# Kernel tuning notes

Hardware: AMD Instinct MI355X
Metric: run time of the kernel (lower is better)

## Reference

```python
import jax, jax.numpy as jnp
import numpy as np

B, S, DIM = 2, 2048, 1024
H, W = 16, 256
HD = DIM // H
SCALE = HD ** -0.5


def setup_inputs() -> dict:
    key = jax.random.key(0)
    ks = jax.random.split(key, 9)
    std = DIM ** -0.5
    return {
        "x": jax.random.normal(ks[0], (B, S, DIM), dtype=jnp.float32),
        "Wq": jax.random.normal(ks[1], (DIM, DIM), dtype=jnp.float32) * std,
        "bq": jnp.zeros((DIM,), dtype=jnp.float32),
        "Wk": jax.random.normal(ks[2], (DIM, DIM), dtype=jnp.float32) * std,
        "bk": jnp.zeros((DIM,), dtype=jnp.float32),
        "Wv": jax.random.normal(ks[3], (DIM, DIM), dtype=jnp.float32) * std,
        "bv": jnp.zeros((DIM,), dtype=jnp.float32),
        "Wo": jax.random.normal(ks[4], (DIM, DIM), dtype=jnp.float32) * std,
        "bo": jnp.zeros((DIM,), dtype=jnp.float32),
    }


def reference(x, Wq, bq, Wk, bk, Wv, bv, Wo, bo):
    b, s, dim = x.shape
    q = (x @ Wq + bq).reshape(b, s, H, HD).transpose(0, 2, 1, 3)  # [B,H,S,HD]
    k = (x @ Wk + bk).reshape(b, s, H, HD).transpose(0, 2, 1, 3)
    v = (x @ Wv + bv).reshape(b, s, H, HD).transpose(0, 2, 1, 3)

    scores = jnp.einsum("bhid,bhjd->bhij", q, k) * SCALE  # [B,H,S,S]
    i = jnp.arange(s)[:, None]
    j = jnp.arange(s)[None, :]
    # valid keys: within causal sliding window [i-W+1, i]
    valid = (j <= i) & (j >= i - W + 1)
    scores = jnp.where(valid, scores, -jnp.inf)
    attn = jax.nn.softmax(scores, axis=-1)
    out = jnp.einsum("bhij,bhjd->bhid", attn, v)  # [B,H,S,HD]
    out = out.transpose(0, 2, 1, 3).reshape(b, s, dim)
    return out @ Wo + bo
```

## Files before the change

kernel.cpp:

```cpp
#include <hip/hip_runtime.h>
#include <stdint.h>

typedef __bf16 bf16;
typedef __bf16 bf16x8 __attribute__((ext_vector_type(8)));
typedef float f32x4 __attribute__((ext_vector_type(4)));

#define MFMA16(a, b, c) __builtin_amdgcn_mfma_f32_16x16x32_bf16((a), (b), (c), 0, 0, 0)

__device__ __forceinline__ void ldsdma16(const void* g, void* l) {
  __builtin_amdgcn_global_load_lds((const __attribute__((address_space(1))) void*)g,
                                   (__attribute__((address_space(3))) void*)l, 16, 0, 0);
}

__global__ __launch_bounds__(256) void prep_kernel(const float* __restrict__ x,
                                                   const float* __restrict__ Wq,
                                                   const float* __restrict__ Wk,
                                                   const float* __restrict__ Wv,
                                                   const float* __restrict__ Wo,
                                                   bf16* __restrict__ xb,
                                                   bf16* __restrict__ WT) {
  __shared__ float tile[64][65];
  if (blockIdx.z == 4) {
    const int t = (blockIdx.y * 16 + blockIdx.x) * 256 + threadIdx.x;
#pragma unroll
    for (int i = 0; i < 16; ++i) {
      const int idx = (t + i * 65536) * 4;
      float4 v = *(const float4*)(x + idx);
      union { bf16 h[4]; uint2 u; } p;
      p.h[0] = (bf16)v.x; p.h[1] = (bf16)v.y; p.h[2] = (bf16)v.z; p.h[3] = (bf16)v.w;
      *(uint2*)(xb + idx) = p.u;
    }
    return;
  }
  const float* src = blockIdx.z == 0 ? Wq : blockIdx.z == 1 ? Wk : blockIdx.z == 2 ? Wv : Wo;
  bf16* dst = WT + (size_t)blockIdx.z * 1024 * 1024;
  const int k0 = blockIdx.y * 64, n0 = blockIdx.x * 64;
  const int rr = threadIdx.x >> 6, c = threadIdx.x & 63;
#pragma unroll
  for (int i = 0; i < 16; ++i) {
    int r = i * 4 + rr;
    tile[r][c] = src[(size_t)(k0 + r) * 1024 + n0 + c];
  }
  __syncthreads();
#pragma unroll
  for (int i = 0; i < 16; ++i) {
    int r = i * 4 + rr;
    dst[(size_t)(n0 + r) * 1024 + k0 + c] = (bf16)tile[c][r];
  }
}

__device__ __forceinline__ void stage_half(const bf16* __restrict__ src, int rowbase,
                                           int koff, char* lds, int bufq, int wave,
                                           int lane) {
#pragma unroll
  for (int i = 0; i < 2; ++i) {
    int chunk = i * 512 + wave * 64 + lane;
    int row = chunk >> 3;
    int cg = (chunk & 7) ^ (row & 7);
    ldsdma16(src + (size_t)(rowbase + row) * 1024 + koff + cg * 8,
             lds + bufq * 16384 + (i * 512 + wave * 64) * 16);
  }
}

__device__ __forceinline__ void ld_frag4(const bf16* lds, int bufq, int rbase, int quad,
                                         int l16, bf16x8 (&d)[4][2]) {
  const bf16x8* hb = (const bf16x8*)lds + bufq * 1024;
#pragma unroll
  for (int mf = 0; mf < 4; ++mf) {
    int row = rbase + mf * 16 + l16;
#pragma unroll
    for (int kk = 0; kk < 2; ++kk)
      d[mf][kk] = hb[row * 8 + ((kk * 4 + quad) ^ (row & 7))];
  }
}

__device__ __forceinline__ void ld_frag2(const bf16* lds, int bufq, int rbase, int quad,
                                         int l16, bf16x8 (&d)[2][2]) {
  const bf16x8* hb = (const bf16x8*)lds + bufq * 1024;
#pragma unroll
  for (int nf = 0; nf < 2; ++nf) {
    int row = rbase + nf * 16 + l16;
#pragma unroll
    for (int kk = 0; kk < 2; ++kk)
      d[nf][kk] = hb[row * 8 + ((kk * 4 + quad) ^ (row & 7))];
  }
}

template <int MQ, int NQ>
__device__ __forceinline__ void mma_quad(f32x4 (&acc)[8][4], const bf16x8 (&a)[4][2],
                                         const bf16x8 (&b)[2][2]) {
  __builtin_amdgcn_s_setprio(1);
#pragma unroll
  for (int mf = 0; mf < 4; ++mf)
#pragma unroll
    for (int nf = 0; nf < 2; ++nf)
#pragma unroll
      for (int kk = 0; kk < 2; ++kk)
        acc[MQ * 4 + mf][NQ * 2 + nf] =
            MFMA16(a[mf][kk], b[nf][kk], acc[MQ * 4 + mf][NQ * 2 + nf]);
  __builtin_amdgcn_s_setprio(0);
}

#define QBAR1() { __builtin_amdgcn_s_barrier(); \
                  asm volatile("s_waitcnt lgkmcnt(0)" ::: "memory"); }
#define QBAR2() { __builtin_amdgcn_s_barrier(); }

template <bool PRE>
__device__ __forceinline__ void qkv_iter(int k0, const bf16* __restrict__ xb,
                                         const bf16* __restrict__ BT, int m0, int n0,
                                         bf16* As, bf16* Bs, f32x4 (&acc)[8][4], int wave,
                                         int lane, int wm, int wn, int quad, int l16) {
  bf16x8 aF[4][2], b0F[2][2], b1F[2][2];
  ld_frag4(As, 0, wm * 64, quad, l16, aF);
  ld_frag2(Bs, 0, wn * 32, quad, l16, b0F);
  stage_half(xb, m0 + 128, k0 + 64, (char*)As, 3, wave, lane);
  QBAR1(); mma_quad<0, 0>(acc, aF, b0F); QBAR2();
  ld_frag2(Bs, 1, wn * 32, quad, l16, b1F);
  stage_half(BT, n0, k0 + 64, (char*)Bs, 2, wave, lane);
  QBAR1(); mma_quad<0, 1>(acc, aF, b1F); QBAR2();
  ld_frag4(As, 1, wm * 64, quad, l16, aF);
  if (PRE) stage_half(xb, m0, k0 + 128, (char*)As, 0, wave, lane);
  QBAR1(); mma_quad<1, 1>(acc, aF, b1F); QBAR2();
  if (PRE) stage_half(BT, n0 + 128, k0 + 128, (char*)Bs, 1, wave, lane);
  QBAR1(); mma_quad<1, 0>(acc, aF, b0F);
  if (PRE) { asm volatile("s_waitcnt vmcnt(4)" ::: "memory"); }
  else     { asm volatile("s_waitcnt vmcnt(0)" ::: "memory"); }
  QBAR2();
  ld_frag4(As, 2, wm * 64, quad, l16, aF);
  ld_frag2(Bs, 2, wn * 32, quad, l16, b0F);
  if (PRE) stage_half(xb, m0 + 128, k0 + 128, (char*)As, 1, wave, lane);
  QBAR1(); mma_quad<0, 0>(acc, aF, b0F); QBAR2();
  ld_frag2(Bs, 3, wn * 32, quad, l16, b1F);
  if (PRE) stage_half(BT, n0, k0 + 128, (char*)Bs, 0, wave, lane);
  QBAR1(); mma_quad<0, 1>(acc, aF, b1F); QBAR2();
  ld_frag4(As, 3, wm * 64, quad, l16, aF);
  if (PRE) stage_half(xb, m0, k0 + 192, (char*)As, 2, wave, lane);
  QBAR1(); mma_quad<1, 1>(acc, aF, b1F); QBAR2();
  if (PRE) stage_half(BT, n0 + 128, k0 + 192, (char*)Bs, 3, wave, lane);
  QBAR1(); mma_quad<1, 0>(acc, aF, b0F);
  if (PRE) { asm volatile("s_waitcnt vmcnt(4)" ::: "memory"); }
  QBAR2();
}

__global__ __launch_bounds__(512, 2) void qkv_gemm8(const bf16* __restrict__ xb,
                                                    const bf16* __restrict__ WT,
                                                    const float* __restrict__ bq,
                                                    const float* __restrict__ bk,
                                                    const float* __restrict__ bv,
                                                    bf16* __restrict__ Qd,
                                                    bf16* __restrict__ Kd,
                                                    bf16* __restrict__ Vd) {
  extern __shared__ char smem_raw[];
  bf16* As = (bf16*)smem_raw;
  bf16* Bs = (bf16*)(smem_raw + 65536);

  const int tid = threadIdx.x, lane = tid & 63, wave = tid >> 6;
  const int wm = wave >> 2, wn = wave & 3;
  const int quad = lane >> 4, l16 = lane & 15;
  const int m0 = blockIdx.y * 256, n0 = blockIdx.x * 256;

  f32x4 acc[8][4];
  const f32x4 zero = {0.f, 0.f, 0.f, 0.f};
#pragma unroll
  for (int i = 0; i < 8; ++i)
#pragma unroll
    for (int j = 0; j < 4; ++j) acc[i][j] = zero;

  stage_half(xb, m0, 0, (char*)As, 0, wave, lane);
  stage_half(WT, n0, 0, (char*)Bs, 0, wave, lane);
  stage_half(xb, m0 + 128, 0, (char*)As, 1, wave, lane);
  stage_half(WT, n0 + 128, 0, (char*)Bs, 1, wave, lane);
  stage_half(xb, m0, 64, (char*)As, 2, wave, lane);
  stage_half(WT, n0 + 128, 64, (char*)Bs, 3, wave, lane);
  asm volatile("s_waitcnt vmcnt(4)" ::: "memory");
  __builtin_amdgcn_s_barrier();

  for (int j = 0; j < 7; ++j)
    qkv_iter<true>(j * 128, xb, WT, m0, n0, As, Bs, acc, wave, lane, wm, wn, quad, l16);
  qkv_iter<false>(896, xb, WT, m0, n0, As, Bs, acc, wave, lane, wm, wn, quad, l16);

#pragma unroll
  for (int MQ = 0; MQ < 2; ++MQ)
#pragma unroll
    for (int mf = 0; mf < 4; ++mf)
#pragma unroll
      for (int NQ = 0; NQ < 2; ++NQ)
#pragma unroll
        for (int nf = 0; nf < 2; ++nf) {
          const int n = n0 + NQ * 128 + wn * 32 + nf * 16 + l16;
          const int sel = n >> 10, d = n & 1023;
          const float bias = (sel == 0 ? bq : sel == 1 ? bk : bv)[d];
          bf16* dst = (sel == 0 ? Qd : sel == 1 ? Kd : Vd);
          const float scl = (sel == 0) ? 0.125f : 1.f;
          const int h = d >> 6, hd = d & 63;
#pragma unroll
          for (int r = 0; r < 4; ++r) {
            const int token = m0 + MQ * 128 + wm * 64 + mf * 16 + quad * 4 + r;
            const int bb = token >> 11, s = token & 2047;
            const float v = (acc[MQ * 4 + mf][NQ * 2 + nf][r] + bias) * scl;
            dst[((((size_t)bb * 16 + h) * 2048 + s) << 6) + hd] = (bf16)v;
          }
        }
}

template <int NJ>
__device__ __forceinline__ void gemm_mainloop(const bf16* __restrict__ A,
                                              const bf16* __restrict__ BT, int K,
                                              int m0, int n0, bf16* As, bf16* Bs,
                                              f32x4 (&acc)[4][NJ]) {
  constexpr int BN = NJ * 32;
  const int tid = threadIdx.x;
  const int lane = tid & 63;
  const int wave = tid >> 6;
  const int wm = wave >> 1, wn = wave & 1;
  const int quad = lane >> 4, l16 = lane & 15;

  const f32x4 zero = {0.f, 0.f, 0.f, 0.f};
#pragma unroll
  for (int i = 0; i < 4; ++i)
#pragma unroll
    for (int j = 0; j < NJ; ++j) acc[i][j] = zero;

  for (int k0 = 0; k0 < K; k0 += 32) {
#pragma unroll
    for (int c = 0; c < 2; ++c) {
      int chunk = wave * 128 + c * 64 + lane;
      int row = chunk >> 2;
      int cg = (chunk & 3) ^ ((row >> 1) & 3);
      ldsdma16(A + (size_t)(m0 + row) * K + k0 + cg * 8,
               (char*)As + (size_t)(wave * 128 + c * 64) * 16);
    }
#pragma unroll
    for (int c = 0; c < BN / 64; ++c) {
      int chunk = wave * (BN / 64) * 64 + c * 64 + lane;
      int row = chunk >> 2;
      int cg = (chunk & 3) ^ ((row >> 1) & 3);
      ldsdma16(BT + (size_t)(n0 + row) * K + k0 + cg * 8,
               (char*)Bs + (size_t)(wave * (BN / 64) * 64 + c * 64) * 16);
    }
    __syncthreads();
    bf16x8 af[4], bfv[NJ];
#pragma unroll
    for (int i = 0; i < 4; ++i) {
      int ra = wm * 64 + i * 16 + l16;
      af[i] = ((const bf16x8*)As)[ra * 4 + (quad ^ ((ra >> 1) & 3))];
    }
#pragma unroll
    for (int j = 0; j < NJ; ++j) {
      int rb = wn * (BN / 2) + j * 16 + l16;
      bfv[j] = ((const bf16x8*)Bs)[rb * 4 + (quad ^ ((rb >> 1) & 3))];
    }
#pragma unroll
    for (int i = 0; i < 4; ++i)
#pragma unroll
      for (int j = 0; j < NJ; ++j) acc[i][j] = MFMA16(af[i], bfv[j], acc[i][j]);
    __syncthreads();
  }
}

template <int NT, int MODE>
__device__ __forceinline__ void attn_phase(const int start, const bf16* __restrict__ Kb,
                                           const bf16* __restrict__ Vb, bf16* Ks, bf16* Vt,
                                           bf16* Psw, const bf16x8 qa0, const bf16x8 qa1,
                                           const int i0, float (&mrow)[4], float (&lrow)[4],
                                           f32x4 (&oacc)[4]) {
  const int tid = threadIdx.x, lane = tid & 63, wave = tid >> 6;
  const int quad = lane >> 4, l16 = lane & 15;
  const f32x4 zero = {0.f, 0.f, 0.f, 0.f};

  __syncthreads();
#pragma unroll
  for (int c = 0; c < NT / 2; ++c) {
    int chunk = c * 256 + wave * 64 + lane;
    int row = chunk >> 3;
    int cg = (chunk & 7) ^ (row & 7);
    ldsdma16(Kb + (size_t)(start + row) * 64 + cg * 8,
             (char*)Ks + (size_t)(c * 256 + wave * 64) * 16);
  }
  if (NT == 8) {
    const int key = tid >> 1, hc = (tid & 1) * 32;
    const bf16* vp = Vb + (size_t)(start + key) * 64 + hc;
    bf16x8 v0 = ((const bf16x8*)vp)[0], v1 = ((const bf16x8*)vp)[1];
    bf16x8 v2 = ((const bf16x8*)vp)[2], v3 = ((const bf16x8*)vp)[3];
#pragma unroll
    for (int i = 0; i < 8; ++i) Vt[(hc + i) * 136 + key] = v0[i];
#pragma unroll
    for (int i = 0; i < 8; ++i) Vt[(hc + 8 + i) * 136 + key] = v1[i];
#pragma unroll
    for (int i = 0; i < 8; ++i) Vt[(hc + 16 + i) * 136 + key] = v2[i];
#pragma unroll
    for (int i = 0; i < 8; ++i) Vt[(hc + 24 + i) * 136 + key] = v3[i];
  } else {
    const int key = tid >> 2, hc = (tid & 3) * 16;
    const bf16* vp = Vb + (size_t)(start + key) * 64 + hc;
    bf16x8 v0 = ((const bf16x8*)vp)[0], v1 = ((const bf16x8*)vp)[1];
#pragma unroll
    for (int i = 0; i < 8; ++i) Vt[(hc + i) * 136 + key] = v0[i];
#pragma unroll
    for (int i = 0; i < 8; ++i) Vt[(hc + 8 + i) * 136 + key] = v1[i];
  }
  __syncthreads();

  f32x4 sc[NT];
  __builtin_amdgcn_s_setprio(1);
#pragma unroll
  for (int nt = 0; nt < NT; ++nt) {
    int key = nt * 16 + l16;
    bf16x8 kb0 = ((const bf16x8*)Ks)[key * 8 + ((0 * 4 + quad) ^ (key & 7))];
    bf16x8 kb1 = ((const bf16x8*)Ks)[key * 8 + ((1 * 4 + quad) ^ (key & 7))];
    f32x4 s = zero;
    s = MFMA16(qa0, kb0, s);
    s = MFMA16(qa1, kb1, s);
    sc[nt] = s;
  }
  __builtin_amdgcn_s_setprio(0);

  float alpha[4];
#pragma unroll
  for (int r = 0; r < 4; ++r) {
    const int i = i0 + r;
    float mx = -1e30f;
#pragma unroll
    for (int nt = 0; nt < NT; ++nt) {
      float s = sc[nt][r];
      if (MODE == 1) {
        const bool valid = (start + nt * 16 + l16 + 255 >= i);
        s = valid ? s : -1e30f;
        sc[nt][r] = s;
      } else if (MODE == 2) {
        const bool valid = (start + nt * 16 + l16 <= i);
        s = valid ? s : -1e30f;
        sc[nt][r] = s;
      }
      mx = fmaxf(mx, s);
    }
#pragma unroll
    for (int m = 8; m >= 1; m >>= 1) mx = fmaxf(mx, __shfl_xor(mx, m, 64));
    const float mnew = fmaxf(mrow[r], mx);
    alpha[r] = __expf(mrow[r] - mnew);
    mrow[r] = mnew;
    float rs = 0.f;
#pragma unroll
    for (int nt = 0; nt < NT; ++nt) {
      const float p = __expf(sc[nt][r] - mnew);
      sc[nt][r] = p;
      rs += p;
    }
#pragma unroll
    for (int m = 8; m >= 1; m >>= 1) rs += __shfl_xor(rs, m, 64);
    lrow[r] = lrow[r] * alpha[r] + rs;
  }

#pragma unroll
  for (int nt = 0; nt < NT; ++nt)
#pragma unroll
    for (int r = 0; r < 4; ++r)
      Psw[(quad * 4 + r) * 136 + nt * 16 + l16] = (bf16)sc[nt][r];
  asm volatile("s_waitcnt lgkmcnt(0)" ::: "memory");
  bf16x8 pa[NT / 2];
#pragma unroll
  for (int ks = 0; ks < NT / 2; ++ks)
    pa[ks] = ((const bf16x8*)Psw)[l16 * 17 + ks * 4 + quad];

  __builtin_amdgcn_s_setprio(1);
#pragma unroll
  for (int ht = 0; ht < 4; ++ht) {
    f32x4 o = oacc[ht];
#pragma unroll
    for (int r = 0; r < 4; ++r) o[r] *= alpha[r];
#pragma unroll
    for (int ks = 0; ks < NT / 2; ++ks) {
      bf16x8 vb = ((const bf16x8*)Vt)[(ht * 16 + l16) * 17 + ks * 4 + quad];
      o = MFMA16(pa[ks], vb, o);
    }
    oacc[ht] = o;
  }
  __builtin_amdgcn_s_setprio(0);
}

__global__ __launch_bounds__(256) void attn_kernel(const bf16* __restrict__ Q,
                                                   const bf16* __restrict__ K,
                                                   const bf16* __restrict__ V,
                                                   bf16* __restrict__ Ao) {
  __shared__ bf16 Ks[128 * 64] __attribute__((aligned(16)));
  __shared__ bf16 Vt[64 * 136] __attribute__((aligned(16)));
  __shared__ bf16 Ps[4][16 * 136] __attribute__((aligned(16)));

  const int tid = threadIdx.x, lane = tid & 63, wave = tid >> 6;
  const int quad = lane >> 4, l16 = lane & 15;
  const int qt = blockIdx.x, h = blockIdx.y, b = blockIdx.z;
  const int q0 = qt * 64;
  const size_t base = ((size_t)(b * 16 + h)) * 2048 * 64;
  const bf16* Qb = Q + base + (size_t)q0 * 64;
  const bf16* Kb = K + base;
  const bf16* Vb = V + base;

  const bf16* qrow = Qb + (size_t)(wave * 16 + l16) * 64 + quad * 8;
  const bf16x8 qa0 = *(const bf16x8*)qrow;
  const bf16x8 qa1 = *(const bf16x8*)(qrow + 32);

  float mrow[4], lrow[4];
  f32x4 oacc[4];
  const f32x4 zero = {0.f, 0.f, 0.f, 0.f};
#pragma unroll
  for (int r = 0; r < 4; ++r) { mrow[r] = -1e30f; lrow[r] = 0.f; }
#pragma unroll
  for (int t = 0; t < 4; ++t) oacc[t] = zero;

  const int i0 = q0 + wave * 16 + quad * 4;
  bf16* Psw = Ps[wave];

  if (q0 >= 256)
    attn_phase<8, 1>(q0 - 256, Kb, Vb, Ks, Vt, Psw, qa0, qa1, i0, mrow, lrow, oacc);
  else if (q0 == 192)
    attn_phase<4, 0>(0, Kb, Vb, Ks, Vt, Psw, qa0, qa1, i0, mrow, lrow, oacc);
  if (q0 >= 128)
    attn_phase<8, 0>(q0 - 128, Kb, Vb, Ks, Vt, Psw, qa0, qa1, i0, mrow, lrow, oacc);
  else if (q0 == 64)
    attn_phase<4, 0>(0, Kb, Vb, Ks, Vt, Psw, qa0, qa1, i0, mrow, lrow, oacc);
  attn_phase<4, 2>(q0, Kb, Vb, Ks, Vt, Psw, qa0, qa1, i0, mrow, lrow, oacc);

#pragma unroll
  for (int r = 0; r < 4; ++r) {
    const float inv = 1.f / lrow[r];
    const int row = q0 + wave * 16 + quad * 4 + r;
    const size_t outb = ((size_t)(b * 2048 + row)) * 1024 + h * 64;
#pragma unroll
    for (int ht = 0; ht < 4; ++ht)
      Ao[outb + ht * 16 + l16] = (bf16)(oacc[ht][r] * inv);
  }
}

__global__ __launch_bounds__(256) void out_gemm(const bf16* __restrict__ Ain,
                                                const bf16* __restrict__ WoT,
                                                const float* __restrict__ bo,
                                                float* __restrict__ out) {
  __shared__ bf16 As[128 * 32] __attribute__((aligned(16)));
  __shared__ bf16 Bs[64 * 32] __attribute__((aligned(16)));
  f32x4 acc[4][2];
  const int m0 = blockIdx.y * 128, n0 = blockIdx.x * 64;
  gemm_mainloop<2>(Ain, WoT, 1024, m0, n0, As, Bs, acc);

  const int lane = threadIdx.x & 63, wave = threadIdx.x >> 6;
  const int wm = wave >> 1, wn = wave & 1;
  const int quad = lane >> 4, l16 = lane & 15;
#pragma unroll
  for (int j = 0; j < 2; ++j) {
    const int n = n0 + wn * 32 + j * 16 + l16;
    const float bias = bo[n];
#pragma unroll
    for (int i = 0; i < 4; ++i) {
#pragma unroll
      for (int r = 0; r < 4; ++r) {
        const int token = m0 + wm * 64 + i * 16 + quad * 4 + r;
        out[(size_t)token * 1024 + n] = acc[i][j][r] + bias;
      }
    }
  }
}

extern "C" void kernel_launch(void* const* d_in, const int* in_sizes, int n_in,
                              void* d_out, int out_size, void* d_ws, size_t ws_size,
                              hipStream_t stream) {
  const float* x  = (const float*)d_in[0];
  const float* Wq = (const float*)d_in[1];
  const float* bq = (const float*)d_in[2];
  const float* Wk = (const float*)d_in[3];
  const float* bk = (const float*)d_in[4];
  const float* Wv = (const float*)d_in[5];
  const float* bv = (const float*)d_in[6];
  const float* Wo = (const float*)d_in[7];
  const float* bo = (const float*)d_in[8];
  float* out = (float*)d_out;

  char* ws = (char*)d_ws;
  bf16* xb = (bf16*)(ws);
  bf16* WT = (bf16*)(ws + ((size_t)8 << 20));
  bf16* Qd = (bf16*)(ws + ((size_t)16 << 20));
  bf16* Kd = (bf16*)(ws + ((size_t)24 << 20));
  bf16* Vd = (bf16*)(ws + ((size_t)32 << 20));
  bf16* Ao = (bf16*)(ws + ((size_t)40 << 20));

  (void)hipFuncSetAttribute((const void*)qkv_gemm8,
                            hipFuncAttributeMaxDynamicSharedMemorySize, 131072);

  prep_kernel<<<dim3(16, 16, 5), 256, 0, stream>>>(x, Wq, Wk, Wv, Wo, xb, WT);
  qkv_gemm8<<<dim3(12, 16), 512, 131072, stream>>>(xb, WT, bq, bk, bv, Qd, Kd, Vd);
  attn_kernel<<<dim3(32, 16, 2), 256, 0, stream>>>(Qd, Kd, Vd, Ao);
  out_gemm<<<dim3(16, 32), 256, 0, stream>>>(Ao, WT + (size_t)3 * 1024 * 1024, bo, out);
}
```

Measured before the change: 169.1 us.

## Fuse all four stages into one persistent cooperative kernel with grid barriers

Replaces the four separate launches (prep/convert, QKV GEMM, sliding-window attention, output GEMM) with a single persistent kernel of 256 blocks of 512 threads. Stages are separated by atomic-counter grid barriers. Attention is reorganised into 128-query jobs, two per block, with only full 128-key phases. The output GEMM is re-tiled to 128x128 with 64-wide K steps. This removes launch gaps and tail effects between kernels. The cost is that idle blocks wait at grid barriers, the QKV stage uses only 192 of the 256 blocks, and the fallback non-cooperative launch risks deadlock if not all blocks are co-resident.

```diff
diff --git a/kernel.cpp b/kernel.cpp
--- a/kernel.cpp
+++ b/kernel.cpp
@@ -12,41 +12,15 @@
                                    (__attribute__((address_space(3))) void*)l, 16, 0, 0);
 }
 
-__global__ __launch_bounds__(256) void prep_kernel(const float* __restrict__ x,
-                                                   const float* __restrict__ Wq,
-                                                   const float* __restrict__ Wk,
-                                                   const float* __restrict__ Wv,
-                                                   const float* __restrict__ Wo,
-                                                   bf16* __restrict__ xb,
-                                                   bf16* __restrict__ WT) {
-  __shared__ float tile[64][65];
-  if (blockIdx.z == 4) {
-    const int t = (blockIdx.y * 16 + blockIdx.x) * 256 + threadIdx.x;
-#pragma unroll
-    for (int i = 0; i < 16; ++i) {
-      const int idx = (t + i * 65536) * 4;
-      float4 v = *(const float4*)(x + idx);
-      union { bf16 h[4]; uint2 u; } p;
-      p.h[0] = (bf16)v.x; p.h[1] = (bf16)v.y; p.h[2] = (bf16)v.z; p.h[3] = (bf16)v.w;
-      *(uint2*)(xb + idx) = p.u;
-    }
-    return;
-  }
-  const float* src = blockIdx.z == 0 ? Wq : blockIdx.z == 1 ? Wk : blockIdx.z == 2 ? Wv : Wo;
-  bf16* dst = WT + (size_t)blockIdx.z * 1024 * 1024;
-  const int k0 = blockIdx.y * 64, n0 = blockIdx.x * 64;
-  const int rr = threadIdx.x >> 6, c = threadIdx.x & 63;
-#pragma unroll
-  for (int i = 0; i < 16; ++i) {
-    int r = i * 4 + rr;
-    tile[r][c] = src[(size_t)(k0 + r) * 1024 + n0 + c];
-  }
+__device__ __forceinline__ void gridbar(unsigned* cnt, unsigned target) {
   __syncthreads();
-#pragma unroll
-  for (int i = 0; i < 16; ++i) {
-    int r = i * 4 + rr;
-    dst[(size_t)(n0 + r) * 1024 + k0 + c] = (bf16)tile[c][r];
-  }
+  if (threadIdx.x == 0) {
+    __hip_atomic_fetch_add(cnt, 1u, __ATOMIC_ACQ_REL, __HIP_MEMORY_SCOPE_AGENT);
+    while (__hip_atomic_load(cnt, __ATOMIC_RELAXED, __HIP_MEMORY_SCOPE_AGENT) < target)
+      __builtin_amdgcn_s_sleep(8);
+    (void)__hip_atomic_load(cnt, __ATOMIC_ACQUIRE, __HIP_MEMORY_SCOPE_AGENT);
+  }
+  __syncthreads();
 }
 
 __device__ __forceinline__ void stage_half(const bf16* __restrict__ src, int rowbase,
@@ -142,155 +116,26 @@
   QBAR2();
 }
 
-__global__ __launch_bounds__(512, 2) void qkv_gemm8(const bf16* __restrict__ xb,
-                                                    const bf16* __restrict__ WT,
-                                                    const float* __restrict__ bq,
-                                                    const float* __restrict__ bk,
-                                                    const float* __restrict__ bv,
-                                                    bf16* __restrict__ Qd,
-                                                    bf16* __restrict__ Kd,
-                                                    bf16* __restrict__ Vd) {
-  extern __shared__ char smem_raw[];
-  bf16* As = (bf16*)smem_raw;
-  bf16* Bs = (bf16*)(smem_raw + 65536);
-
-  const int tid = threadIdx.x, lane = tid & 63, wave = tid >> 6;
-  const int wm = wave >> 2, wn = wave & 3;
-  const int quad = lane >> 4, l16 = lane & 15;
-  const int m0 = blockIdx.y * 256, n0 = blockIdx.x * 256;
-
-  f32x4 acc[8][4];
-  const f32x4 zero = {0.f, 0.f, 0.f, 0.f};
-#pragma unroll
-  for (int i = 0; i < 8; ++i)
-#pragma unroll
-    for (int j = 0; j < 4; ++j) acc[i][j] = zero;
-
-  stage_half(xb, m0, 0, (char*)As, 0, wave, lane);
-  stage_half(WT, n0, 0, (char*)Bs, 0, wave, lane);
-  stage_half(xb, m0 + 128, 0, (char*)As, 1, wave, lane);
-  stage_half(WT, n0 + 128, 0, (char*)Bs, 1, wave, lane);
-  stage_half(xb, m0, 64, (char*)As, 2, wave, lane);
-  stage_half(WT, n0 + 128, 64, (char*)Bs, 3, wave, lane);
-  asm volatile("s_waitcnt vmcnt(4)" ::: "memory");
-  __builtin_amdgcn_s_barrier();
-
-  for (int j = 0; j < 7; ++j)
-    qkv_iter<true>(j * 128, xb, WT, m0, n0, As, Bs, acc, wave, lane, wm, wn, quad, l16);
-  qkv_iter<false>(896, xb, WT, m0, n0, As, Bs, acc, wave, lane, wm, wn, quad, l16);
-
-#pragma unroll
-  for (int MQ = 0; MQ < 2; ++MQ)
-#pragma unroll
-    for (int mf = 0; mf < 4; ++mf)
-#pragma unroll
-      for (int NQ = 0; NQ < 2; ++NQ)
-#pragma unroll
-        for (int nf = 0; nf < 2; ++nf) {
-          const int n = n0 + NQ * 128 + wn * 32 + nf * 16 + l16;
-          const int sel = n >> 10, d = n & 1023;
-          const float bias = (sel == 0 ? bq : sel == 1 ? bk : bv)[d];
-          bf16* dst = (sel == 0 ? Qd : sel == 1 ? Kd : Vd);
-          const float scl = (sel == 0) ? 0.125f : 1.f;
-          const int h = d >> 6, hd = d & 63;
-#pragma unroll
-          for (int r = 0; r < 4; ++r) {
-            const int token = m0 + MQ * 128 + wm * 64 + mf * 16 + quad * 4 + r;
-            const int bb = token >> 11, s = token & 2047;
-            const float v = (acc[MQ * 4 + mf][NQ * 2 + nf][r] + bias) * scl;
-            dst[((((size_t)bb * 16 + h) * 2048 + s) << 6) + hd] = (bf16)v;
-          }
-        }
-}
-
-template <int NJ>
-__device__ __forceinline__ void gemm_mainloop(const bf16* __restrict__ A,
-                                              const bf16* __restrict__ BT, int K,
-                                              int m0, int n0, bf16* As, bf16* Bs,
-                                              f32x4 (&acc)[4][NJ]) {
-  constexpr int BN = NJ * 32;
-  const int tid = threadIdx.x;
-  const int lane = tid & 63;
-  const int wave = tid >> 6;
-  const int wm = wave >> 1, wn = wave & 1;
-  const int quad = lane >> 4, l16 = lane & 15;
-
-  const f32x4 zero = {0.f, 0.f, 0.f, 0.f};
-#pragma unroll
-  for (int i = 0; i < 4; ++i)
-#pragma unroll
-    for (int j = 0; j < NJ; ++j) acc[i][j] = zero;
-
-  for (int k0 = 0; k0 < K; k0 += 32) {
-#pragma unroll
-    for (int c = 0; c < 2; ++c) {
-      int chunk = wave * 128 + c * 64 + lane;
-      int row = chunk >> 2;
-      int cg = (chunk & 3) ^ ((row >> 1) & 3);
-      ldsdma16(A + (size_t)(m0 + row) * K + k0 + cg * 8,
-               (char*)As + (size_t)(wave * 128 + c * 64) * 16);
-    }
-#pragma unroll
-    for (int c = 0; c < BN / 64; ++c) {
-      int chunk = wave * (BN / 64) * 64 + c * 64 + lane;
-      int row = chunk >> 2;
-      int cg = (chunk & 3) ^ ((row >> 1) & 3);
-      ldsdma16(BT + (size_t)(n0 + row) * K + k0 + cg * 8,
-               (char*)Bs + (size_t)(wave * (BN / 64) * 64 + c * 64) * 16);
-    }
-    __syncthreads();
-    bf16x8 af[4], bfv[NJ];
-#pragma unroll
-    for (int i = 0; i < 4; ++i) {
-      int ra = wm * 64 + i * 16 + l16;
-      af[i] = ((const bf16x8*)As)[ra * 4 + (quad ^ ((ra >> 1) & 3))];
-    }
-#pragma unroll
-    for (int j = 0; j < NJ; ++j) {
-      int rb = wn * (BN / 2) + j * 16 + l16;
-      bfv[j] = ((const bf16x8*)Bs)[rb * 4 + (quad ^ ((rb >> 1) & 3))];
-    }
-#pragma unroll
-    for (int i = 0; i < 4; ++i)
-#pragma unroll
-      for (int j = 0; j < NJ; ++j) acc[i][j] = MFMA16(af[i], bfv[j], acc[i][j]);
-    __syncthreads();
-  }
-}
-
-template <int NT, int MODE>
-__device__ __forceinline__ void attn_phase(const int start, const bf16* __restrict__ Kb,
-                                           const bf16* __restrict__ Vb, bf16* Ks, bf16* Vt,
-                                           bf16* Psw, const bf16x8 qa0, const bf16x8 qa1,
-                                           const int i0, float (&mrow)[4], float (&lrow)[4],
-                                           f32x4 (&oacc)[4]) {
+template <int MODE>
+__device__ __forceinline__ void attn_phase8(int start, const bf16* __restrict__ Kb,
+                                            const bf16* __restrict__ Vb, bf16* Ks, bf16* Vt,
+                                            bf16* Psw, const bf16x8 qa0, const bf16x8 qa1,
+                                            int i0, float (&mrow)[4], float (&lrow)[4],
+                                            f32x4 (&oacc)[4]) {
   const int tid = threadIdx.x, lane = tid & 63, wave = tid >> 6;
   const int quad = lane >> 4, l16 = lane & 15;
   const f32x4 zero = {0.f, 0.f, 0.f, 0.f};
 
   __syncthreads();
 #pragma unroll
-  for (int c = 0; c < NT / 2; ++c) {
-    int chunk = c * 256 + wave * 64 + lane;
+  for (int c = 0; c < 2; ++c) {
+    int chunk = c * 512 + wave * 64 + lane;
     int row = chunk >> 3;
     int cg = (chunk & 7) ^ (row & 7);
     ldsdma16(Kb + (size_t)(start + row) * 64 + cg * 8,
-             (char*)Ks + (size_t)(c * 256 + wave * 64) * 16);
-  }
-  if (NT == 8) {
-    const int key = tid >> 1, hc = (tid & 1) * 32;
-    const bf16* vp = Vb + (size_t)(start + key) * 64 + hc;
-    bf16x8 v0 = ((const bf16x8*)vp)[0], v1 = ((const bf16x8*)vp)[1];
-    bf16x8 v2 = ((const bf16x8*)vp)[2], v3 = ((const bf16x8*)vp)[3];
-#pragma unroll
-    for (int i = 0; i < 8; ++i) Vt[(hc + i) * 136 + key] = v0[i];
-#pragma unroll
-    for (int i = 0; i < 8; ++i) Vt[(hc + 8 + i) * 136 + key] = v1[i];
-#pragma unroll
-    for (int i = 0; i < 8; ++i) Vt[(hc + 16 + i) * 136 + key] = v2[i];
-#pragma unroll
-    for (int i = 0; i < 8; ++i) Vt[(hc + 24 + i) * 136 + key] = v3[i];
-  } else {
+             (char*)Ks + (size_t)(c * 512 + wave * 64) * 16);
+  }
+  {
     const int key = tid >> 2, hc = (tid & 3) * 16;
     const bf16* vp = Vb + (size_t)(start + key) * 64 + hc;
     bf16x8 v0 = ((const bf16x8*)vp)[0], v1 = ((const bf16x8*)vp)[1];
@@ -301,10 +146,10 @@
   }
   __syncthreads();
 
-  f32x4 sc[NT];
+  f32x4 sc[8];
   __builtin_amdgcn_s_setprio(1);
 #pragma unroll
-  for (int nt = 0; nt < NT; ++nt) {
+  for (int nt = 0; nt < 8; ++nt) {
     int key = nt * 16 + l16;
     bf16x8 kb0 = ((const bf16x8*)Ks)[key * 8 + ((0 * 4 + quad) ^ (key & 7))];
     bf16x8 kb1 = ((const bf16x8*)Ks)[key * 8 + ((1 * 4 + quad) ^ (key & 7))];
@@ -321,7 +166,7 @@
     const int i = i0 + r;
     float mx = -1e30f;
 #pragma unroll
-    for (int nt = 0; nt < NT; ++nt) {
+    for (int nt = 0; nt < 8; ++nt) {
       float s = sc[nt][r];
       if (MODE == 1) {
         const bool valid = (start + nt * 16 + l16 + 255 >= i);
@@ -341,7 +186,7 @@
     mrow[r] = mnew;
     float rs = 0.f;
 #pragma unroll
-    for (int nt = 0; nt < NT; ++nt) {
+    for (int nt = 0; nt < 8; ++nt) {
       const float p = __expf(sc[nt][r] - mnew);
       sc[nt][r] = p;
       rs += p;
@@ -352,14 +197,14 @@
   }
 
 #pragma unroll
-  for (int nt = 0; nt < NT; ++nt)
+  for (int nt = 0; nt < 8; ++nt)
 #pragma unroll
     for (int r = 0; r < 4; ++r)
       Psw[(quad * 4 + r) * 136 + nt * 16 + l16] = (bf16)sc[nt][r];
   asm volatile("s_waitcnt lgkmcnt(0)" ::: "memory");
-  bf16x8 pa[NT / 2];
-#pragma unroll
-  for (int ks = 0; ks < NT / 2; ++ks)
+  bf16x8 pa[4];
+#pragma unroll
+  for (int ks = 0; ks < 4; ++ks)
     pa[ks] = ((const bf16x8*)Psw)[l16 * 17 + ks * 4 + quad];
 
   __builtin_amdgcn_s_setprio(1);
@@ -369,7 +214,7 @@
 #pragma unroll
     for (int r = 0; r < 4; ++r) o[r] *= alpha[r];
 #pragma unroll
-    for (int ks = 0; ks < NT / 2; ++ks) {
+    for (int ks = 0; ks < 4; ++ks) {
       bf16x8 vb = ((const bf16x8*)Vt)[(ht * 16 + l16) * 17 + ks * 4 + quad];
       o = MFMA16(pa[ks], vb, o);
     }
@@ -378,18 +223,14 @@
   __builtin_amdgcn_s_setprio(0);
 }
 
-__global__ __launch_bounds__(256) void attn_kernel(const bf16* __restrict__ Q,
-                                                   const bf16* __restrict__ K,
-                                                   const bf16* __restrict__ V,
-                                                   bf16* __restrict__ Ao) {
-  __shared__ bf16 Ks[128 * 64] __attribute__((aligned(16)));
-  __shared__ bf16 Vt[64 * 136] __attribute__((aligned(16)));
-  __shared__ bf16 Ps[4][16 * 136] __attribute__((aligned(16)));
-
+__device__ __forceinline__ void attn_job(int job, const bf16* __restrict__ Q,
+                                         const bf16* __restrict__ K,
+                                         const bf16* __restrict__ V, bf16* __restrict__ Ao,
+                                         bf16* Ks, bf16* Vt, bf16* Ps) {
   const int tid = threadIdx.x, lane = tid & 63, wave = tid >> 6;
   const int quad = lane >> 4, l16 = lane & 15;
-  const int qt = blockIdx.x, h = blockIdx.y, b = blockIdx.z;
-  const int q0 = qt * 64;
+  const int qt = job & 15, h = (job >> 4) & 15, b = job >> 8;
+  const int q0 = qt * 128;
   const size_t base = ((size_t)(b * 16 + h)) * 2048 * 64;
   const bf16* Qb = Q + base + (size_t)q0 * 64;
   const bf16* Kb = K + base;
@@ -408,17 +249,13 @@
   for (int t = 0; t < 4; ++t) oacc[t] = zero;
 
   const int i0 = q0 + wave * 16 + quad * 4;
-  bf16* Psw = Ps[wave];
+  bf16* Psw = Ps + wave * (16 * 136);
 
   if (q0 >= 256)
-    attn_phase<8, 1>(q0 - 256, Kb, Vb, Ks, Vt, Psw, qa0, qa1, i0, mrow, lrow, oacc);
-  else if (q0 == 192)
-    attn_phase<4, 0>(0, Kb, Vb, Ks, Vt, Psw, qa0, qa1, i0, mrow, lrow, oacc);
+    attn_phase8<1>(q0 - 256, Kb, Vb, Ks, Vt, Psw, qa0, qa1, i0, mrow, lrow, oacc);
   if (q0 >= 128)
-    attn_phase<8, 0>(q0 - 128, Kb, Vb, Ks, Vt, Psw, qa0, qa1, i0, mrow, lrow, oacc);
-  else if (q0 == 64)
-    attn_phase<4, 0>(0, Kb, Vb, Ks, Vt, Psw, qa0, qa1, i0, mrow, lrow, oacc);
-  attn_phase<4, 2>(q0, Kb, Vb, Ks, Vt, Psw, qa0, qa1, i0, mrow, lrow, oacc);
+    attn_phase8<0>(q0 - 128, Kb, Vb, Ks, Vt, Psw, qa0, qa1, i0, mrow, lrow, oacc);
+  attn_phase8<2>(q0, Kb, Vb, Ks, Vt, Psw, qa0, qa1, i0, mrow, lrow, oacc);
 
 #pragma unroll
   for (int r = 0; r < 4; ++r) {
@@ -431,29 +268,169 @@
   }
 }
 
-__global__ __launch_bounds__(256) void out_gemm(const bf16* __restrict__ Ain,
-                                                const bf16* __restrict__ WoT,
-                                                const float* __restrict__ bo,
-                                                float* __restrict__ out) {
-  __shared__ bf16 As[128 * 32] __attribute__((aligned(16)));
-  __shared__ bf16 Bs[64 * 32] __attribute__((aligned(16)));
-  f32x4 acc[4][2];
-  const int m0 = blockIdx.y * 128, n0 = blockIdx.x * 64;
-  gemm_mainloop<2>(Ain, WoT, 1024, m0, n0, As, Bs, acc);
-
-  const int lane = threadIdx.x & 63, wave = threadIdx.x >> 6;
-  const int wm = wave >> 1, wn = wave & 1;
+__global__ void __launch_bounds__(512, 2)
+mega(const float* __restrict__ x, const float* __restrict__ Wq,
+     const float* __restrict__ Wk, const float* __restrict__ Wv,
+     const float* __restrict__ Wo, const float* __restrict__ bq,
+     const float* __restrict__ bk, const float* __restrict__ bv,
+     const float* __restrict__ bo, bf16* __restrict__ xb, bf16* __restrict__ WT,
+     bf16* __restrict__ Qd, bf16* __restrict__ Kd, bf16* __restrict__ Vd,
+     bf16* __restrict__ Ao, float* __restrict__ out, unsigned* cnt) {
+  extern __shared__ char smem[];
+  const int tid = threadIdx.x, lane = tid & 63, wave = tid >> 6;
   const int quad = lane >> 4, l16 = lane & 15;
-#pragma unroll
-  for (int j = 0; j < 2; ++j) {
-    const int n = n0 + wn * 32 + j * 16 + l16;
-    const float bias = bo[n];
-#pragma unroll
-    for (int i = 0; i < 4; ++i) {
-#pragma unroll
-      for (int r = 0; r < 4; ++r) {
-        const int token = m0 + wm * 64 + i * 16 + quad * 4 + r;
-        out[(size_t)token * 1024 + n] = acc[i][j][r] + bias;
+  const int bid = blockIdx.x;
+
+  {
+    const int gt = bid * 512 + tid;
+#pragma unroll
+    for (int it = 0; it < 8; ++it) {
+      const int i4 = it * 131072 + gt;
+      const float4 v = ((const float4*)x)[i4];
+      union { bf16 h[4]; uint2 u; } p;
+      p.h[0] = (bf16)v.x; p.h[1] = (bf16)v.y; p.h[2] = (bf16)v.z; p.h[3] = (bf16)v.w;
+      ((uint2*)xb)[i4] = p.u;
+    }
+    float (*tile)[65] = (float (*)[65])smem;
+    const int rr = tid >> 6, c = tid & 63;
+    for (int tj = 0; tj < 4; ++tj) {
+      const int id = bid * 4 + tj;
+      const int mat = id >> 8;
+      const float* src = mat == 0 ? Wq : mat == 1 ? Wk : mat == 2 ? Wv : Wo;
+      bf16* dst = WT + (size_t)mat * 1048576;
+      const int k0 = ((id >> 4) & 15) * 64, n0 = (id & 15) * 64;
+      __syncthreads();
+#pragma unroll
+      for (int i2 = 0; i2 < 8; ++i2) {
+        const int r = i2 * 8 + rr;
+        tile[r][c] = src[(size_t)(k0 + r) * 1024 + n0 + c];
+      }
+      __syncthreads();
+#pragma unroll
+      for (int i2 = 0; i2 < 8; ++i2) {
+        const int r = i2 * 8 + rr;
+        dst[(size_t)(n0 + r) * 1024 + k0 + c] = (bf16)tile[c][r];
+      }
+    }
+  }
+  gridbar(cnt, 256);
+
+  if (bid < 192) {
+    bf16* As = (bf16*)smem;
+    bf16* Bs = (bf16*)(smem + 65536);
+    const int m0 = (bid / 12) * 256, n0 = (bid % 12) * 256;
+    const int wm = wave >> 2, wn = wave & 3;
+
+    f32x4 acc[8][4];
+    const f32x4 zero = {0.f, 0.f, 0.f, 0.f};
+#pragma unroll
+    for (int i = 0; i < 8; ++i)
+#pragma unroll
+      for (int j = 0; j < 4; ++j) acc[i][j] = zero;
+
+    stage_half(xb, m0, 0, (char*)As, 0, wave, lane);
+    stage_half(WT, n0, 0, (char*)Bs, 0, wave, lane);
+    stage_half(xb, m0 + 128, 0, (char*)As, 1, wave, lane);
+    stage_half(WT, n0 + 128, 0, (char*)Bs, 1, wave, lane);
+    stage_half(xb, m0, 64, (char*)As, 2, wave, lane);
+    stage_half(WT, n0 + 128, 64, (char*)Bs, 3, wave, lane);
+    asm volatile("s_waitcnt vmcnt(4)" ::: "memory");
+    __builtin_amdgcn_s_barrier();
+
+    for (int j = 0; j < 7; ++j)
+      qkv_iter<true>(j * 128, xb, WT, m0, n0, As, Bs, acc, wave, lane, wm, wn, quad, l16);
+    qkv_iter<false>(896, xb, WT, m0, n0, As, Bs, acc, wave, lane, wm, wn, quad, l16);
+
+#pragma unroll
+    for (int MQ = 0; MQ < 2; ++MQ)
+#pragma unroll
+      for (int mf = 0; mf < 4; ++mf)
+#pragma unroll
+        for (int NQ = 0; NQ < 2; ++NQ)
+#pragma unroll
+          for (int nf = 0; nf < 2; ++nf) {
+            const int n = n0 + NQ * 128 + wn * 32 + nf * 16 + l16;
+            const int sel = n >> 10, d = n & 1023;
+            const float bias = (sel == 0 ? bq : sel == 1 ? bk : bv)[d];
+            bf16* dst = (sel == 0 ? Qd : sel == 1 ? Kd : Vd);
+            const float scl = (sel == 0) ? 0.125f : 1.f;
+            const int h = d >> 6, hd = d & 63;
+#pragma unroll
+            for (int r = 0; r < 4; ++r) {
+              const int token = m0 + MQ * 128 + wm * 64 + mf * 16 + quad * 4 + r;
+              const int bb = token >> 11, s = token & 2047;
+              const float v = (acc[MQ * 4 + mf][NQ * 2 + nf][r] + bias) * scl;
+              dst[((((size_t)bb * 16 + h) * 2048 + s) << 6) + hd] = (bf16)v;
+            }
+          }
+  }
+  gridbar(cnt, 512);
+
+  {
+    bf16* Ks = (bf16*)smem;
+    bf16* Vt = (bf16*)(smem + 16384);
+    bf16* Ps = (bf16*)(smem + 33792);
+    attn_job(bid, Qd, Kd, Vd, Ao, Ks, Vt, Ps);
+    attn_job(bid + 256, Qd, Kd, Vd, Ao, Ks, Vt, Ps);
+  }
+  gridbar(cnt, 768);
+
+  {
+    bf16* As = (bf16*)smem;
+    bf16* Bs = (bf16*)(smem + 16384);
+    const bf16* WoT = WT + (size_t)3 * 1048576;
+    const int m0 = (bid >> 3) * 128, n0 = (bid & 7) * 128;
+    const int wm = wave >> 2, wn = wave & 3;
+
+    f32x4 acc[4][2];
+    const f32x4 zero = {0.f, 0.f, 0.f, 0.f};
+#pragma unroll
+    for (int i = 0; i < 4; ++i)
+#pragma unroll
+      for (int j = 0; j < 2; ++j) acc[i][j] = zero;
+
+    for (int k0 = 0; k0 < 1024; k0 += 64) {
+#pragma unroll
+      for (int i = 0; i < 2; ++i) {
+        const int chunk = i * 512 + wave * 64 + lane;
+        const int row = chunk >> 3, cg = (chunk & 7) ^ (row & 7);
+        ldsdma16(Ao + (size_t)(m0 + row) * 1024 + k0 + cg * 8,
+                 (char*)As + (size_t)(i * 512 + wave * 64) * 16);
+      }
+#pragma unroll
+      for (int i = 0; i < 2; ++i) {
+        const int chunk = i * 512 + wave * 64 + lane;
+        const int row = chunk >> 3, cg = (chunk & 7) ^ (row & 7);
+        ldsdma16(WoT + (size_t)(n0 + row) * 1024 + k0 + cg * 8,
+                 (char*)Bs + (size_t)(i * 512 + wave * 64) * 16);
+      }
+      __syncthreads();
+      bf16x8 aF[4][2], bF[2][2];
+      ld_frag4(As, 0, wm * 64, quad, l16, aF);
+      ld_frag2(Bs, 0, wn * 32, quad, l16, bF);
+      __builtin_amdgcn_s_setprio(1);
+#pragma unroll
+      for (int mf = 0; mf < 4; ++mf)
+#pragma unroll
+        for (int nf = 0; nf < 2; ++nf)
+#pragma unroll
+          for (int kk = 0; kk < 2; ++kk)
+            acc[mf][nf] = MFMA16(aF[mf][kk], bF[nf][kk], acc[mf][nf]);
+      __builtin_amdgcn_s_setprio(0);
+      __syncthreads();
+    }
+
+#pragma unroll
+    for (int nf = 0; nf < 2; ++nf) {
+      const int n = n0 + wn * 32 + nf * 16 + l16;
+      const float bias = bo[n];
+#pragma unroll
+      for (int mf = 0; mf < 4; ++mf) {
+#pragma unroll
+        for (int r = 0; r < 4; ++r) {
+          const int token = m0 + wm * 64 + mf * 16 + quad * 4 + r;
+          out[(size_t)token * 1024 + n] = acc[mf][nf][r] + bias;
+        }
       }
     }
   }
@@ -471,7 +448,7 @@
   const float* bv = (const float*)d_in[6];
   const float* Wo = (const float*)d_in[7];
   const float* bo = (const float*)d_in[8];
-  float* out = (float*)d_out;
+  float* outp = (float*)d_out;
 
   char* ws = (char*)d_ws;
   bf16* xb = (bf16*)(ws);
@@ -480,12 +457,20 @@
   bf16* Kd = (bf16*)(ws + ((size_t)24 << 20));
   bf16* Vd = (bf16*)(ws + ((size_t)32 << 20));
   bf16* Ao = (bf16*)(ws + ((size_t)40 << 20));
-
-  (void)hipFuncSetAttribute((const void*)qkv_gemm8,
+  unsigned* cnt = (unsigned*)(ws + ((size_t)48 << 20));
+
+  (void)hipFuncSetAttribute((const void*)mega,
                             hipFuncAttributeMaxDynamicSharedMemorySize, 131072);
-
-  prep_kernel<<<dim3(16, 16, 5), 256, 0, stream>>>(x, Wq, Wk, Wv, Wo, xb, WT);
-  qkv_gemm8<<<dim3(12, 16), 512, 131072, stream>>>(xb, WT, bq, bk, bv, Qd, Kd, Vd);
-  attn_kernel<<<dim3(32, 16, 2), 256, 0, stream>>>(Qd, Kd, Vd, Ao);
-  out_gemm<<<dim3(16, 32), 256, 0, stream>>>(Ao, WT + (size_t)3 * 1024 * 1024, bo, out);
-}
+  (void)hipMemsetAsync(cnt, 0, 256, stream);
+
+  void* kargs[] = {(void*)&x,  (void*)&Wq, (void*)&Wk, (void*)&Wv, (void*)&Wo,
+                   (void*)&bq, (void*)&bk, (void*)&bv, (void*)&bo,
+                   (void*)&xb, (void*)&WT, (void*)&Qd, (void*)&Kd, (void*)&Vd,
+                   (void*)&Ao, (void*)&outp, (void*)&cnt};
+  hipError_t err = hipLaunchCooperativeKernel((const void*)mega, dim3(256), dim3(512),
+                                              kargs, 131072, stream);
+  if (err != hipSuccess) {
+    mega<<<dim3(256), dim3(512), 131072, stream>>>(x, Wq, Wk, Wv, Wo, bq, bk, bv, bo,
+                                                   xb, WT, Qd, Kd, Vd, Ao, outp, cnt);
+  }
+}
```

New measurement: 267.4 us. 58.1% more time.
